# Optimization experiments

Measured on AMD Instinct MI355X. Metric: run time of the kernel, lower is better.

Reference implementation:

```python
import jax, jax.numpy as jnp
import numpy as np

D_MODEL = 1024
N_HEADS = 16
HEAD_DIM = D_MODEL // N_HEADS
LN_EPS = 1e-6


def setup_inputs() -> dict:
    key = jax.random.key(0)
    ks = jax.random.split(key, 10)
    B, L, D = 4, 1024, D_MODEL
    s = 1.0 / np.sqrt(D)
    return {
        "q": jax.random.normal(ks[0], (B, L, D), jnp.float32),
        "k": jax.random.normal(ks[1], (B, L, D), jnp.float32),
        "v": jax.random.normal(ks[2], (B, L, D), jnp.float32),
        "masks": jnp.zeros((B, L, L), jnp.bool_),
        "Wq": jax.random.normal(ks[3], (D, D), jnp.float32) * s,
        "bq": jnp.zeros((D,), jnp.float32),
        "Wk": jax.random.normal(ks[4], (D, D), jnp.float32) * s,
        "bk": jnp.zeros((D,), jnp.float32),
        "Wv": jax.random.normal(ks[5], (D, D), jnp.float32) * s,
        "bv": jnp.zeros((D,), jnp.float32),
        "ln_g": jnp.ones((D,), jnp.float32),
        "ln_b": jnp.zeros((D,), jnp.float32),
    }


def _layer_norm(x, g, b):
    mu = jnp.mean(x, axis=-1, keepdims=True)
    var = jnp.var(x, axis=-1, keepdims=True)
    return (x - mu) * jax.lax.rsqrt(var + LN_EPS) * g + b


def reference(q, k, v, masks, Wq, bq, Wk, bk, Wv, bv, ln_g, ln_b):
    B, Lq, D = q.shape
    Lk = k.shape[1]
    H, Dh = N_HEADS, HEAD_DIM
    # linear projections (nn.Linear: x @ W.T + b)
    qp = q @ Wq.T + bq  # [B, Lq, D]
    kp = k @ Wk.T + bk
    vp = v @ Wv.T + bv
    # split heads: [B, L, D] -> [B, H, L, Dh]
    qh = qp.reshape(B, Lq, H, Dh).transpose(0, 2, 1, 3)
    kh = kp.reshape(B, Lk, H, Dh).transpose(0, 2, 1, 3)
    vh = vp.reshape(B, Lk, H, Dh).transpose(0, 2, 1, 3)
    scores = jnp.einsum("bhqd,bhkd->bhqk", qh, kh) / jnp.sqrt(jnp.float32(Dh))
    scores = jnp.where(masks[:, None, :, :], -jnp.inf, scores)
    attention = jax.nn.softmax(scores, axis=-1)  # [B, H, Lq, Lk]
    ctx = jnp.einsum("bhqk,bhkd->bhqd", attention, vh)  # [B, H, Lq, Dh]
    ctx = ctx.transpose(0, 2, 1, 3).reshape(B, Lq, D)  # unmulti_head
    output = _layer_norm(qp + ctx, ln_g, ln_b)  # residual is projected q
    return output, attention.reshape(B * H, Lq, Lk)
```

## Files before the change

kernel.cpp:

```cpp
#include <hip/hip_runtime.h>
#include <hip/hip_bf16.h>

typedef short bf16x8 __attribute__((ext_vector_type(8)));
typedef short bf16x4 __attribute__((ext_vector_type(4)));
typedef float f32x4 __attribute__((ext_vector_type(4)));
typedef unsigned short u16x8 __attribute__((ext_vector_type(8)));
typedef unsigned short u16x4 __attribute__((ext_vector_type(4)));

#define DEV static __device__ __forceinline__

DEV unsigned short f2bf(float f) {
  unsigned int u = __builtin_bit_cast(unsigned int, f);
  u += 0x7FFFu + ((u >> 16) & 1u);
  return (unsigned short)(u >> 16);
}
DEV float bf2f(unsigned short u) {
  return __builtin_bit_cast(float, (unsigned int)u << 16);
}

DEV void gload_lds16(const unsigned short* g, unsigned short* l) {
  __builtin_amdgcn_global_load_lds(
      (const __attribute__((address_space(1))) unsigned int*)g,
      (__attribute__((address_space(3))) unsigned int*)l, 16, 0, 0);
}

DEV void waitv(int n) {
  switch (n) {
    case 0: asm volatile("s_waitcnt vmcnt(0)" ::: "memory"); break;
    case 1: asm volatile("s_waitcnt vmcnt(1)" ::: "memory"); break;
    case 2: asm volatile("s_waitcnt vmcnt(2)" ::: "memory"); break;
    case 4: asm volatile("s_waitcnt vmcnt(4)" ::: "memory"); break;
    case 6: asm volatile("s_waitcnt vmcnt(6)" ::: "memory"); break;
    default: asm volatile("s_waitcnt vmcnt(0)" ::: "memory"); break;
  }
}

#define SB() __builtin_amdgcn_sched_barrier(0)
#define BAR() do { __builtin_amdgcn_s_barrier(); SB(); } while (0)
#define LBAR() do { asm volatile("s_waitcnt lgkmcnt(0)" ::: "memory"); \
                    SB(); \
                    __builtin_amdgcn_s_barrier(); \
                    SB(); } while (0)
#define WAITL() do { asm volatile("s_waitcnt lgkmcnt(0)" ::: "memory"); SB(); } while (0)
#define PRIO1() __builtin_amdgcn_s_setprio(1)
#define PRIO0() __builtin_amdgcn_s_setprio(0)

__global__ __launch_bounds__(256) void cvt_kernel(
    const float* __restrict__ q, const float* __restrict__ k,
    const float* __restrict__ v, const float* __restrict__ wq,
    const float* __restrict__ wk, const float* __restrict__ wv,
    unsigned short* __restrict__ xq, unsigned short* __restrict__ xk,
    unsigned short* __restrict__ xv, unsigned short* __restrict__ wqb,
    unsigned short* __restrict__ wkb, unsigned short* __restrict__ wvb)
{
  int tid = blockIdx.x * 256 + threadIdx.x;
  const float* src; unsigned short* dst; int off;
  if      (tid <  524288) { src = q;  dst = xq;  off = tid; }
  else if (tid < 1048576) { src = k;  dst = xk;  off = tid -  524288; }
  else if (tid < 1572864) { src = v;  dst = xv;  off = tid - 1048576; }
  else if (tid < 1703936) { src = wq; dst = wqb; off = tid - 1572864; }
  else if (tid < 1835008) { src = wk; dst = wkb; off = tid - 1703936; }
  else                    { src = wv; dst = wvb; off = tid - 1835008; }
  size_t e = (size_t)off * 8;
  float4 a = *(const float4*)(src + e);
  float4 b = *(const float4*)(src + e + 4);
  u16x8 p = { f2bf(a.x), f2bf(a.y), f2bf(a.z), f2bf(a.w),
              f2bf(b.x), f2bf(b.y), f2bf(b.z), f2bf(b.w) };
  *(u16x8*)(dst + e) = p;
}

__global__ __launch_bounds__(512, 2) void gemm_kernel(
    const unsigned short* __restrict__ xq, const unsigned short* __restrict__ xk,
    const unsigned short* __restrict__ xv, const unsigned short* __restrict__ wqb,
    const unsigned short* __restrict__ wkb, const unsigned short* __restrict__ wvb,
    const float* __restrict__ bq, const float* __restrict__ bk,
    const float* __restrict__ bv, unsigned short* __restrict__ qp,
    unsigned short* __restrict__ kp, unsigned short* __restrict__ vt)
{
  __shared__ union {
    unsigned short ab[2][2][128][64];
    unsigned short T[128][132];
  } smu;
  const int t = threadIdx.x, lane = t & 63, wv8 = t >> 6;
  const int ln = lane & 15, g = lane >> 4;
  const int wm2 = wv8 >> 2, wn4 = wv8 & 3;
  const int seg = blockIdx.x >> 8, lb = blockIdx.x & 255;
  const int x8 = lb & 7, s32 = lb >> 3;
  const int m0 = (x8 * 4 + (s32 >> 3)) * 128;
  const int n0 = (s32 & 7) * 128;

  const unsigned short* X; const unsigned short* W; const float* bias;
  unsigned short* outR; int mode;
  if (seg == 0)      { X = xq; W = wqb; bias = bq; outR = qp; mode = 0; }
  else if (seg == 1) { X = xk; W = wkb; bias = bk; outR = kp; mode = 0; }
  else               { X = xv; W = wvb; bias = bv; outR = vt; mode = 2; }

  f32x4 acc[4][2];
#pragma unroll
  for (int i = 0; i < 4; ++i)
#pragma unroll
    for (int j = 0; j < 2; ++j) acc[i][j] = {0.f, 0.f, 0.f, 0.f};

  const int lrow = lane >> 3;
  const int lcol = ((lane & 7) ^ lrow) * 8;

#define STAGE_G(kt) do { \
    const int _k0 = (kt) * 64; \
    _Pragma("unroll") \
    for (int i = 0; i < 2; ++i) { \
      const int r = wv8 * 16 + i * 8; \
      gload_lds16(X + (size_t)(m0 + r + lrow) * 1024 + _k0 + lcol, \
                  &smu.ab[(kt) & 1][0][r][0]); \
      gload_lds16(W + (size_t)(n0 + r + lrow) * 1024 + _k0 + lcol, \
                  &smu.ab[(kt) & 1][1][r][0]); \
    } } while (0)

  STAGE_G(0);
  waitv(0);
  BAR();
#pragma unroll 2
  for (int kt = 0; kt < 16; ++kt) {
    if (kt < 15) STAGE_G(kt + 1);
    SB();
#pragma unroll
    for (int ks = 0; ks < 2; ++ks) {
      bf16x8 af[4], bfr[2];
      const int ru = ((ks * 4 + g) ^ (ln & 7)) * 8;
#pragma unroll
      for (int i = 0; i < 4; ++i)
        af[i] = *(const bf16x8*)&smu.ab[kt & 1][0][wm2 * 64 + i * 16 + ln][ru];
#pragma unroll
      for (int j = 0; j < 2; ++j)
        bfr[j] = *(const bf16x8*)&smu.ab[kt & 1][1][wn4 * 32 + j * 16 + ln][ru];
      PRIO1();
#pragma unroll
      for (int i = 0; i < 4; ++i)
#pragma unroll
        for (int j = 0; j < 2; ++j)
          acc[i][j] = __builtin_amdgcn_mfma_f32_16x16x32_bf16(
              af[i], bfr[j], acc[i][j], 0, 0, 0);
      PRIO0();
    }
    SB();
    waitv(0);
    BAR();
  }

  float bvv[2];
#pragma unroll
  for (int j = 0; j < 2; ++j) bvv[j] = bias[n0 + wn4 * 32 + j * 16 + ln];

  if (mode == 0) {
#pragma unroll
    for (int i = 0; i < 4; ++i)
#pragma unroll
      for (int j = 0; j < 2; ++j)
#pragma unroll
        for (int r = 0; r < 4; ++r) {
          int row = m0 + wm2 * 64 + i * 16 + g * 4 + r;
          int col = n0 + wn4 * 32 + j * 16 + ln;
          outR[(size_t)row * 1024 + col] = f2bf(acc[i][j][r] + bvv[j]);
        }
  } else {
    __syncthreads();
#pragma unroll
    for (int i = 0; i < 4; ++i)
#pragma unroll
      for (int j = 0; j < 2; ++j)
#pragma unroll
        for (int r = 0; r < 4; ++r)
          smu.T[wn4 * 32 + j * 16 + ln][wm2 * 64 + i * 16 + g * 4 + r] =
              f2bf(acc[i][j][r] + bvv[j]);
    __syncthreads();
    const int bb = m0 >> 10, l0 = m0 & 1023;
#pragma unroll
    for (int it = 0; it < 4; ++it) {
      const int col = it * 32 + (t >> 4);
      const int r8 = (t & 15) * 8;
      *(u16x8*)&outR[((size_t)(bb * 16 + (n0 >> 6) + (col >> 6)) * 64 + (col & 63)) * 1024 + l0 + r8] =
          *(const u16x8*)&smu.T[col][r8];
    }
  }
#undef STAGE_G
}

__global__ __launch_bounds__(512, 2) void attn_kernel(
    const unsigned short* __restrict__ qp, const unsigned short* __restrict__ kp,
    const unsigned short* __restrict__ vt, const unsigned char* __restrict__ masks,
    float* __restrict__ attn_out, float* __restrict__ res_out)
{
  __shared__ union {
    unsigned short Kw[8][3][1024];
    unsigned short Vb[3][64][128];
    float ctxp[4][32][68];
  } sm;
  __shared__ float red[2][2][16][4];

  const int t = threadIdx.x;
  const int wv = t >> 6, lane = t & 63;
  const int ln = lane & 15, g = lane >> 4;
  const int wq = wv & 3, wm = wv >> 2;
  const int hw = blockIdx.x;
  const int lid = (hw & 7) * 256 + (hw >> 3);
  const int b = lid >> 9, h = (lid >> 5) & 15, m0 = (lid & 31) * 32;
  const size_t rowbase = (size_t)(b * 1024 + m0);

  bf16x8 qf[2];
  {
    const unsigned short* qb =
        qp + (rowbase + wm * 16 + ln) * 1024 + h * 64 + g * 8;
    qf[0] = *(const bf16x8*)qb;
    qf[1] = *(const bf16x8*)(qb + 32);
  }
  SB();

  const int slr8 = lane >> 3;
  const int suK = (lane & 7) ^ slr8;
  const int vlr = lane >> 4;
  const int vu1 = (lane & 15) ^ vlr;
  const int vu2 = (lane & 15) ^ (4 + vlr);
  const unsigned short* kbase = kp + (size_t)b * 1048576 + h * 64;
  const unsigned short* vtb = vt + ((size_t)(b * 16 + h) * 64) * 1024;
  unsigned short* kwv = &sm.Kw[wv][0][0];

#define STAGE_K(tt) do { \
    gload_lds16(kbase + (size_t)((tt) * 64 + wq * 16 + slr8) * 1024 + suK * 8, \
                kwv + ((tt) % 3) * 1024); \
    gload_lds16(kbase + (size_t)((tt) * 64 + wq * 16 + 8 + slr8) * 1024 + suK * 8, \
                kwv + ((tt) % 3) * 1024 + 512); } while (0)
#define STAGE_V(c) do { \
    gload_lds16(vtb + (size_t)(wv * 8 + vlr) * 1024 + (c) * 128 + vu1 * 8, \
                &sm.Vb[(c) % 3][wv * 8][0]); \
    gload_lds16(vtb + (size_t)(wv * 8 + 4 + vlr) * 1024 + (c) * 128 + vu2 * 8, \
                &sm.Vb[(c) % 3][wv * 8 + 4][0]); } while (0)

  f32x4 sc[16];
#pragma unroll
  for (int i = 0; i < 16; ++i) sc[i] = {0.f, 0.f, 0.f, 0.f};

  STAGE_K(0); STAGE_K(1); STAGE_K(2);
  SB();
#pragma unroll
  for (int tt = 0; tt < 16; ++tt) {
    waitv(tt <= 13 ? 4 : (tt == 14 ? 2 : 0));
    SB();
    const unsigned short* ksl = kwv + (tt % 3) * 1024 + ln * 64;
    bf16x8 kf0 = *(const bf16x8*)(ksl + (g ^ (ln & 7)) * 8);
    bf16x8 kf1 = *(const bf16x8*)(ksl + ((4 + g) ^ (ln & 7)) * 8);
    WAITL();
    if (tt + 3 < 16) STAGE_K(tt + 3);
    SB();
    PRIO1();
    sc[tt] = __builtin_amdgcn_mfma_f32_16x16x32_bf16(kf0, qf[0], sc[tt], 0, 0, 0);
    sc[tt] = __builtin_amdgcn_mfma_f32_16x16x32_bf16(kf1, qf[1], sc[tt], 0, 0, 0);
    PRIO0();
  }

  unsigned mw[16];
  {
    const unsigned char* mrow =
        masks + ((size_t)b * 1024 + m0 + wm * 16 + ln) * 1024 + wq * 16 + g * 4;
#pragma unroll
    for (int tt = 0; tt < 16; ++tt) mw[tt] = *(const unsigned*)(mrow + tt * 64);
  }
  SB();

  LBAR();
  STAGE_V(0); STAGE_V(1);
  SB();

  const float C = 0.18033688011112042f;
  float mx = -3.0e30f;
#pragma unroll
  for (int tt = 0; tt < 16; ++tt) {
    if (mw[tt]) {
#pragma unroll
      for (int r = 0; r < 4; ++r)
        if ((mw[tt] >> (8 * r)) & 0xffu) sc[tt][r] = -1.0e30f;
    }
#pragma unroll
    for (int r = 0; r < 4; ++r) mx = fmaxf(mx, sc[tt][r]);
  }
  mx = fmaxf(mx, __shfl_xor(mx, 16));
  mx = fmaxf(mx, __shfl_xor(mx, 32));
  const float mtl = mx * C;
  float sum = 0.f;
#pragma unroll
  for (int tt = 0; tt < 16; ++tt)
#pragma unroll
    for (int r = 0; r < 4; ++r)
      sum += exp2f(__builtin_fmaf(sc[tt][r], C, -mtl));
  sum += __shfl_xor(sum, 16);
  sum += __shfl_xor(sum, 32);
  if (g == 0) { red[0][wm][ln][wq] = mx; red[1][wm][ln][wq] = sum; }
  LBAR();
  float m4 = fmaxf(fmaxf(red[0][wm][ln][0], red[0][wm][ln][1]),
                   fmaxf(red[0][wm][ln][2], red[0][wm][ln][3]));
  float l4 = 0.f;
#pragma unroll
  for (int i = 0; i < 4; ++i)
    l4 += red[1][wm][ln][i] * exp2f((red[0][wm][ln][i] - m4) * C);
  const float beta = __builtin_fmaf(-m4, C, -__builtin_log2f(l4));

  bf16x8 af8[8];
#pragma unroll
  for (int c = 0; c < 8; ++c) {
    bf16x8 a;
#pragma unroll
    for (int r = 0; r < 4; ++r)
      a[r] = (short)f2bf(exp2f(__builtin_fmaf(sc[2 * c][r], C, beta)));
#pragma unroll
    for (int r = 0; r < 4; ++r)
      a[4 + r] = (short)f2bf(exp2f(__builtin_fmaf(sc[2 * c + 1][r], C, beta)));
    af8[c] = a;
  }

  f32x4 cacc[4];
#pragma unroll
  for (int i = 0; i < 4; ++i) cacc[i] = {0.f, 0.f, 0.f, 0.f};
  const size_t abase =
      ((size_t)(b * 16 + h) * 1024 + (m0 + wm * 16 + ln)) * 1024 + wq * 16 + g * 4;
#pragma unroll
  for (int c = 0; c < 8; ++c) {
    waitv(c == 0 ? 2 : (c == 1 ? 4 : (c <= 6 ? 6 : 4)));
    BAR();
    if (c + 2 < 8) STAGE_V(c + 2);
    SB();
#pragma unroll
    for (int ni = 0; ni < 4; ++ni) {
      const int d = ni * 16 + ln;
      const int u0 = (2 * wq + (g >> 1)) ^ (ln & 7);
      const int u1 = (8 + 2 * wq + (g >> 1)) ^ (ln & 7);
      bf16x4 b0 = *(const bf16x4*)&sm.Vb[c % 3][d][u0 * 8 + (g & 1) * 4];
      bf16x4 b1 = *(const bf16x4*)&sm.Vb[c % 3][d][u1 * 8 + (g & 1) * 4];
      bf16x8 bfr = { b0[0], b0[1], b0[2], b0[3], b1[0], b1[1], b1[2], b1[3] };
      PRIO1();
      cacc[ni] = __builtin_amdgcn_mfma_f32_16x16x32_bf16(af8[c], bfr, cacc[ni], 0, 0, 0);
      PRIO0();
    }
    SB();
#pragma unroll
    for (int hf = 0; hf < 2; ++hf) {
      f32x4 v = { bf2f((unsigned short)af8[c][hf * 4 + 0]),
                  bf2f((unsigned short)af8[c][hf * 4 + 1]),
                  bf2f((unsigned short)af8[c][hf * 4 + 2]),
                  bf2f((unsigned short)af8[c][hf * 4 + 3]) };
      *(f32x4*)(attn_out + abase + (2 * c + hf) * 64) = v;
    }
    SB();
  }

  LBAR();
#pragma unroll
  for (int ni = 0; ni < 4; ++ni)
#pragma unroll
    for (int r = 0; r < 4; ++r)
      sm.ctxp[wq][wm * 16 + g * 4 + r][ni * 16 + ln] = cacc[ni][r];
  LBAR();
  {
    const int m = t >> 4, d4 = (t & 15) * 4;
    f32x4 s0 = *(const f32x4*)&sm.ctxp[0][m][d4];
    f32x4 s1 = *(const f32x4*)&sm.ctxp[1][m][d4];
    f32x4 s2 = *(const f32x4*)&sm.ctxp[2][m][d4];
    f32x4 s3 = *(const f32x4*)&sm.ctxp[3][m][d4];
    f32x4 s = s0 + s1 + s2 + s3;
    const unsigned short* qrow = qp + (rowbase + m) * 1024 + h * 64 + d4;
    u16x4 qv = *(const u16x4*)qrow;
    f32x4 qf32 = { bf2f(qv[0]), bf2f(qv[1]), bf2f(qv[2]), bf2f(qv[3]) };
    s = s + qf32;
    *(f32x4*)(res_out + (rowbase + m) * 1024 + h * 64 + d4) = s;
  }
#undef STAGE_K
#undef STAGE_V
}

__global__ __launch_bounds__(256) void ln_kernel(
    float* __restrict__ io,
    const float* __restrict__ gma, const float* __restrict__ bta)
{
  __shared__ float rbuf[2][4];
  const int r = blockIdx.x, t = threadIdx.x;
  const int i4 = t * 4;
  const size_t base = (size_t)r * 1024 + i4;
  f32x4 x = *(const f32x4*)(io + base);
  float s = x[0] + x[1] + x[2] + x[3];
  float q = x[0]*x[0] + x[1]*x[1] + x[2]*x[2] + x[3]*x[3];
#pragma unroll
  for (int off = 1; off < 64; off <<= 1) {
    s += __shfl_xor(s, off);
    q += __shfl_xor(q, off);
  }
  const int wv = t >> 6;
  if ((t & 63) == 0) { rbuf[0][wv] = s; rbuf[1][wv] = q; }
  __syncthreads();
  s = rbuf[0][0] + rbuf[0][1] + rbuf[0][2] + rbuf[0][3];
  q = rbuf[1][0] + rbuf[1][1] + rbuf[1][2] + rbuf[1][3];
  float mu = s * (1.0f / 1024.0f);
  float var = q * (1.0f / 1024.0f) - mu * mu;
  float is = rsqrtf(var + 1e-6f);
  f32x4 gv = *(const f32x4*)(gma + i4);
  f32x4 bv = *(const f32x4*)(bta + i4);
  f32x4 o;
#pragma unroll
  for (int k = 0; k < 4; ++k) o[k] = (x[k] - mu) * is * gv[k] + bv[k];
  *(f32x4*)(io + base) = o;
}

extern "C" void kernel_launch(void* const* d_in, const int* in_sizes, int n_in,
                              void* d_out, int out_size, void* d_ws, size_t ws_size,
                              hipStream_t stream) {
  const float* q  = (const float*)d_in[0];
  const float* k  = (const float*)d_in[1];
  const float* v  = (const float*)d_in[2];
  const unsigned char* masks = (const unsigned char*)d_in[3];
  const float* Wq = (const float*)d_in[4];
  const float* bq = (const float*)d_in[5];
  const float* Wk = (const float*)d_in[6];
  const float* bk = (const float*)d_in[7];
  const float* Wv = (const float*)d_in[8];
  const float* bv = (const float*)d_in[9];
  const float* lg = (const float*)d_in[10];
  const float* lb = (const float*)d_in[11];

  float* out = (float*)d_out;
  float* attn_out = out + (size_t)4 * 1024 * 1024;

  unsigned short* xq  = (unsigned short*)attn_out;
  unsigned short* xk  = xq + 4194304;
  unsigned short* xv  = xk + 4194304;
  unsigned short* wqb = xv + 4194304;
  unsigned short* wkb = wqb + 1048576;
  unsigned short* wvb = wkb + 1048576;

  unsigned short* qp = (unsigned short*)d_ws;
  unsigned short* kp = qp + 4194304;
  unsigned short* vt = kp + 4194304;

  hipLaunchKernelGGL(cvt_kernel, dim3(7680), dim3(256), 0, stream,
                     q, k, v, Wq, Wk, Wv, xq, xk, xv, wqb, wkb, wvb);
  hipLaunchKernelGGL(gemm_kernel, dim3(768), dim3(512), 0, stream,
                     xq, xk, xv, wqb, wkb, wvb, bq, bk, bv, qp, kp, vt);
  hipLaunchKernelGGL(attn_kernel, dim3(2048), dim3(512), 0, stream,
                     qp, kp, vt, masks, attn_out, out);
  hipLaunchKernelGGL(ln_kernel, dim3(4096), dim3(256), 0, stream,
                     out, lg, lb);
}
```

Baseline: 176.5 us.

## Repartition attention: 16-row blocks, 8 waves split keys, per-wave K/V staging

```diff
diff --git a/kernel.cpp b/kernel.cpp
--- a/kernel.cpp
+++ b/kernel.cpp
@@ -29,7 +29,9 @@
     case 0: asm volatile("s_waitcnt vmcnt(0)" ::: "memory"); break;
     case 1: asm volatile("s_waitcnt vmcnt(1)" ::: "memory"); break;
     case 2: asm volatile("s_waitcnt vmcnt(2)" ::: "memory"); break;
+    case 3: asm volatile("s_waitcnt vmcnt(3)" ::: "memory"); break;
     case 4: asm volatile("s_waitcnt vmcnt(4)" ::: "memory"); break;
+    case 5: asm volatile("s_waitcnt vmcnt(5)" ::: "memory"); break;
     case 6: asm volatile("s_waitcnt vmcnt(6)" ::: "memory"); break;
     default: asm volatile("s_waitcnt vmcnt(0)" ::: "memory"); break;
   }
@@ -44,6 +46,14 @@
 #define WAITL() do { asm volatile("s_waitcnt lgkmcnt(0)" ::: "memory"); SB(); } while (0)
 #define PRIO1() __builtin_amdgcn_s_setprio(1)
 #define PRIO0() __builtin_amdgcn_s_setprio(0)
+
+DEV void amask(unsigned mwv, f32x4& s) {
+  if (mwv) {
+#pragma unroll
+    for (int r = 0; r < 4; ++r)
+      if ((mwv >> (8 * r)) & 0xffu) s[r] = -1.0e30f;
+  }
+}
 
 __global__ __launch_bounds__(256) void cvt_kernel(
     const float* __restrict__ q, const float* __restrict__ k,
@@ -184,31 +194,29 @@
 #undef STAGE_G
 }
 
-__global__ __launch_bounds__(512, 2) void attn_kernel(
+__global__ __launch_bounds__(512, 8) void attn_kernel(
     const unsigned short* __restrict__ qp, const unsigned short* __restrict__ kp,
     const unsigned short* __restrict__ vt, const unsigned char* __restrict__ masks,
     float* __restrict__ attn_out, float* __restrict__ res_out)
 {
   __shared__ union {
-    unsigned short Kw[8][3][1024];
-    unsigned short Vb[3][64][128];
-    float ctxp[4][32][68];
+    unsigned short Kw[8][2][1024];
+    unsigned short Vw[8][3][1024];
+    float ctxp[8][16][68];
   } sm;
-  __shared__ float red[2][2][16][4];
+  __shared__ float red[2][16][8];
 
   const int t = threadIdx.x;
-  const int wv = t >> 6, lane = t & 63;
+  const int wq = t >> 6, lane = t & 63;
   const int ln = lane & 15, g = lane >> 4;
-  const int wq = wv & 3, wm = wv >> 2;
   const int hw = blockIdx.x;
-  const int lid = (hw & 7) * 256 + (hw >> 3);
-  const int b = lid >> 9, h = (lid >> 5) & 15, m0 = (lid & 31) * 32;
+  const int lid = (hw & 7) * 512 + (hw >> 3);
+  const int b = lid >> 10, h = (lid >> 6) & 15, m0 = (lid & 63) * 16;
   const size_t rowbase = (size_t)(b * 1024 + m0);
 
   bf16x8 qf[2];
   {
-    const unsigned short* qb =
-        qp + (rowbase + wm * 16 + ln) * 1024 + h * 64 + g * 8;
+    const unsigned short* qb = qp + (rowbase + ln) * 1024 + h * 64 + g * 8;
     qf[0] = *(const bf16x8*)qb;
     qf[1] = *(const bf16x8*)(qb + 32);
   }
@@ -216,95 +224,92 @@
 
   const int slr8 = lane >> 3;
   const int suK = (lane & 7) ^ slr8;
-  const int vlr = lane >> 4;
-  const int vu1 = (lane & 15) ^ vlr;
-  const int vu2 = (lane & 15) ^ (4 + vlr);
-  const unsigned short* kbase = kp + (size_t)b * 1048576 + h * 64;
-  const unsigned short* vtb = vt + ((size_t)(b * 16 + h) * 64) * 1024;
-  unsigned short* kwv = &sm.Kw[wv][0][0];
-
-#define STAGE_K(tt) do { \
-    gload_lds16(kbase + (size_t)((tt) * 64 + wq * 16 + slr8) * 1024 + suK * 8, \
-                kwv + ((tt) % 3) * 1024); \
-    gload_lds16(kbase + (size_t)((tt) * 64 + wq * 16 + 8 + slr8) * 1024 + suK * 8, \
-                kwv + ((tt) % 3) * 1024 + 512); } while (0)
-#define STAGE_V(c) do { \
-    gload_lds16(vtb + (size_t)(wv * 8 + vlr) * 1024 + (c) * 128 + vu1 * 8, \
-                &sm.Vb[(c) % 3][wv * 8][0]); \
-    gload_lds16(vtb + (size_t)(wv * 8 + 4 + vlr) * 1024 + (c) * 128 + vu2 * 8, \
-                &sm.Vb[(c) % 3][wv * 8 + 4][0]); } while (0)
-
-  f32x4 sc[16];
-#pragma unroll
-  for (int i = 0; i < 16; ++i) sc[i] = {0.f, 0.f, 0.f, 0.f};
-
-  STAGE_K(0); STAGE_K(1); STAGE_K(2);
+  const int vdr = lane >> 1;
+  const int vk8 = (lane & 1) * 8;
+  const unsigned short* kbase =
+      kp + (size_t)b * 1048576 + h * 64 + (size_t)wq * 128 * 1024;
+  const unsigned short* vtb =
+      vt + ((size_t)(b * 16 + h) * 64) * 1024 + wq * 128;
+  unsigned short* kwv = &sm.Kw[wq][0][0];
+  unsigned short* vwv = &sm.Vw[wq][0][0];
+  const unsigned char* mrow =
+      masks + ((size_t)b * 1024 + m0 + ln) * 1024 + wq * 128 + g * 4;
+
+#define STAGE_K(s) do { \
+    gload_lds16(kbase + (size_t)((s) * 16 + slr8) * 1024 + suK * 8, \
+                kwv + ((s) & 1) * 1024); \
+    gload_lds16(kbase + (size_t)((s) * 16 + 8 + slr8) * 1024 + suK * 8, \
+                kwv + ((s) & 1) * 1024 + 512); } while (0)
+#define STAGE_V(s) do { \
+    gload_lds16(vtb + (size_t)vdr * 1024 + (s) * 16 + vk8, \
+                vwv + ((s) % 3) * 1024); \
+    gload_lds16(vtb + (size_t)(32 + vdr) * 1024 + (s) * 16 + vk8, \
+                vwv + ((s) % 3) * 1024 + 512); } while (0)
+
+  f32x4 sc[8];
+#pragma unroll
+  for (int i = 0; i < 8; ++i) sc[i] = {0.f, 0.f, 0.f, 0.f};
+
+  STAGE_K(0); STAGE_K(1);
   SB();
-#pragma unroll
-  for (int tt = 0; tt < 16; ++tt) {
-    waitv(tt <= 13 ? 4 : (tt == 14 ? 2 : 0));
-    SB();
-    const unsigned short* ksl = kwv + (tt % 3) * 1024 + ln * 64;
+  unsigned mq[2];
+#pragma unroll
+  for (int s = 0; s < 8; ++s) {
+    waitv(s == 0 ? 2 : (s == 7 ? 1 : 3));
+    SB();
+    const unsigned short* ksl = kwv + (s & 1) * 1024 + ln * 64;
     bf16x8 kf0 = *(const bf16x8*)(ksl + (g ^ (ln & 7)) * 8);
     bf16x8 kf1 = *(const bf16x8*)(ksl + ((4 + g) ^ (ln & 7)) * 8);
     WAITL();
-    if (tt + 3 < 16) STAGE_K(tt + 3);
-    SB();
+    if (s + 2 < 8) STAGE_K(s + 2);
+    SB();
+    if (s >= 2) amask(mq[s & 1], sc[s - 2]);
+    mq[s & 1] = *(const unsigned*)(mrow + s * 16);
     PRIO1();
-    sc[tt] = __builtin_amdgcn_mfma_f32_16x16x32_bf16(kf0, qf[0], sc[tt], 0, 0, 0);
-    sc[tt] = __builtin_amdgcn_mfma_f32_16x16x32_bf16(kf1, qf[1], sc[tt], 0, 0, 0);
+    sc[s] = __builtin_amdgcn_mfma_f32_16x16x32_bf16(kf0, qf[0], sc[s], 0, 0, 0);
+    sc[s] = __builtin_amdgcn_mfma_f32_16x16x32_bf16(kf1, qf[1], sc[s], 0, 0, 0);
     PRIO0();
   }
-
-  unsigned mw[16];
-  {
-    const unsigned char* mrow =
-        masks + ((size_t)b * 1024 + m0 + wm * 16 + ln) * 1024 + wq * 16 + g * 4;
-#pragma unroll
-    for (int tt = 0; tt < 16; ++tt) mw[tt] = *(const unsigned*)(mrow + tt * 64);
-  }
+  waitv(0);
   SB();
-
-  LBAR();
-  STAGE_V(0); STAGE_V(1);
-  SB();
+  amask(mq[0], sc[6]);
+  amask(mq[1], sc[7]);
 
   const float C = 0.18033688011112042f;
   float mx = -3.0e30f;
 #pragma unroll
-  for (int tt = 0; tt < 16; ++tt) {
-    if (mw[tt]) {
-#pragma unroll
-      for (int r = 0; r < 4; ++r)
-        if ((mw[tt] >> (8 * r)) & 0xffu) sc[tt][r] = -1.0e30f;
-    }
-#pragma unroll
-    for (int r = 0; r < 4; ++r) mx = fmaxf(mx, sc[tt][r]);
-  }
+  for (int s = 0; s < 8; ++s)
+#pragma unroll
+    for (int r = 0; r < 4; ++r) mx = fmaxf(mx, sc[s][r]);
   mx = fmaxf(mx, __shfl_xor(mx, 16));
   mx = fmaxf(mx, __shfl_xor(mx, 32));
   const float mtl = mx * C;
   float sum = 0.f;
 #pragma unroll
-  for (int tt = 0; tt < 16; ++tt)
+  for (int s = 0; s < 8; ++s)
 #pragma unroll
     for (int r = 0; r < 4; ++r)
-      sum += exp2f(__builtin_fmaf(sc[tt][r], C, -mtl));
+      sum += exp2f(__builtin_fmaf(sc[s][r], C, -mtl));
   sum += __shfl_xor(sum, 16);
   sum += __shfl_xor(sum, 32);
-  if (g == 0) { red[0][wm][ln][wq] = mx; red[1][wm][ln][wq] = sum; }
+  if (g == 0) { red[0][ln][wq] = mx; red[1][ln][wq] = sum; }
   LBAR();
-  float m4 = fmaxf(fmaxf(red[0][wm][ln][0], red[0][wm][ln][1]),
-                   fmaxf(red[0][wm][ln][2], red[0][wm][ln][3]));
+
+  STAGE_V(0); STAGE_V(1); STAGE_V(2);
+  SB();
+
+  float m4 = red[0][ln][0];
+#pragma unroll
+  for (int i = 1; i < 8; ++i) m4 = fmaxf(m4, red[0][ln][i]);
   float l4 = 0.f;
 #pragma unroll
-  for (int i = 0; i < 4; ++i)
-    l4 += red[1][wm][ln][i] * exp2f((red[0][wm][ln][i] - m4) * C);
+  for (int i = 0; i < 8; ++i)
+    l4 += red[1][ln][i] * exp2f((red[0][ln][i] - m4) * C);
   const float beta = __builtin_fmaf(-m4, C, -__builtin_log2f(l4));
 
-  bf16x8 af8[8];
-#pragma unroll
-  for (int c = 0; c < 8; ++c) {
+  bf16x8 af[4];
+#pragma unroll
+  for (int c = 0; c < 4; ++c) {
     bf16x8 a;
 #pragma unroll
     for (int r = 0; r < 4; ++r)
@@ -312,40 +317,46 @@
 #pragma unroll
     for (int r = 0; r < 4; ++r)
       a[4 + r] = (short)f2bf(exp2f(__builtin_fmaf(sc[2 * c + 1][r], C, beta)));
-    af8[c] = a;
+    af[c] = a;
   }
 
   f32x4 cacc[4];
 #pragma unroll
   for (int i = 0; i < 4; ++i) cacc[i] = {0.f, 0.f, 0.f, 0.f};
   const size_t abase =
-      ((size_t)(b * 16 + h) * 1024 + (m0 + wm * 16 + ln)) * 1024 + wq * 16 + g * 4;
-#pragma unroll
-  for (int c = 0; c < 8; ++c) {
-    waitv(c == 0 ? 2 : (c == 1 ? 4 : (c <= 6 ? 6 : 4)));
-    BAR();
-    if (c + 2 < 8) STAGE_V(c + 2);
-    SB();
+      ((size_t)(b * 16 + h) * 1024 + (m0 + ln)) * 1024 + wq * 128 + g * 4;
+#pragma unroll
+  for (int p = 0; p < 4; ++p) {
+    waitv(p == 0 ? 2 : (p == 3 ? 2 : 4));
+    SB();
+    bf16x4 b0[4], b1[4];
 #pragma unroll
     for (int ni = 0; ni < 4; ++ni) {
       const int d = ni * 16 + ln;
-      const int u0 = (2 * wq + (g >> 1)) ^ (ln & 7);
-      const int u1 = (8 + 2 * wq + (g >> 1)) ^ (ln & 7);
-      bf16x4 b0 = *(const bf16x4*)&sm.Vb[c % 3][d][u0 * 8 + (g & 1) * 4];
-      bf16x4 b1 = *(const bf16x4*)&sm.Vb[c % 3][d][u1 * 8 + (g & 1) * 4];
-      bf16x8 bfr = { b0[0], b0[1], b0[2], b0[3], b1[0], b1[1], b1[2], b1[3] };
-      PRIO1();
-      cacc[ni] = __builtin_amdgcn_mfma_f32_16x16x32_bf16(af8[c], bfr, cacc[ni], 0, 0, 0);
-      PRIO0();
+      b0[ni] = *(const bf16x4*)(vwv + ((2 * p) % 3) * 1024 + d * 16 + g * 4);
+      b1[ni] = *(const bf16x4*)(vwv + ((2 * p + 1) % 3) * 1024 + d * 16 + g * 4);
     }
+    WAITL();
+    if (p == 0)      { STAGE_V(3); STAGE_V(4); }
+    else if (p == 1) { STAGE_V(5); STAGE_V(6); }
+    else if (p == 2) { STAGE_V(7); }
+    SB();
+    PRIO1();
+#pragma unroll
+    for (int ni = 0; ni < 4; ++ni) {
+      bf16x8 bfr = { b0[ni][0], b0[ni][1], b0[ni][2], b0[ni][3],
+                     b1[ni][0], b1[ni][1], b1[ni][2], b1[ni][3] };
+      cacc[ni] = __builtin_amdgcn_mfma_f32_16x16x32_bf16(af[p], bfr, cacc[ni], 0, 0, 0);
+    }
+    PRIO0();
     SB();
 #pragma unroll
     for (int hf = 0; hf < 2; ++hf) {
-      f32x4 v = { bf2f((unsigned short)af8[c][hf * 4 + 0]),
-                  bf2f((unsigned short)af8[c][hf * 4 + 1]),
-                  bf2f((unsigned short)af8[c][hf * 4 + 2]),
-                  bf2f((unsigned short)af8[c][hf * 4 + 3]) };
-      *(f32x4*)(attn_out + abase + (2 * c + hf) * 64) = v;
+      f32x4 v = { bf2f((unsigned short)af[p][hf * 4 + 0]),
+                  bf2f((unsigned short)af[p][hf * 4 + 1]),
+                  bf2f((unsigned short)af[p][hf * 4 + 2]),
+                  bf2f((unsigned short)af[p][hf * 4 + 3]) };
+      *(f32x4*)(attn_out + abase + p * 32 + hf * 16) = v;
     }
     SB();
   }
@@ -355,15 +366,13 @@
   for (int ni = 0; ni < 4; ++ni)
 #pragma unroll
     for (int r = 0; r < 4; ++r)
-      sm.ctxp[wq][wm * 16 + g * 4 + r][ni * 16 + ln] = cacc[ni][r];
+      sm.ctxp[wq][g * 4 + r][ni * 16 + ln] = cacc[ni][r];
   LBAR();
-  {
+  if (t < 256) {
     const int m = t >> 4, d4 = (t & 15) * 4;
-    f32x4 s0 = *(const f32x4*)&sm.ctxp[0][m][d4];
-    f32x4 s1 = *(const f32x4*)&sm.ctxp[1][m][d4];
-    f32x4 s2 = *(const f32x4*)&sm.ctxp[2][m][d4];
-    f32x4 s3 = *(const f32x4*)&sm.ctxp[3][m][d4];
-    f32x4 s = s0 + s1 + s2 + s3;
+    f32x4 s = *(const f32x4*)&sm.ctxp[0][m][d4];
+#pragma unroll
+    for (int w = 1; w < 8; ++w) s += *(const f32x4*)&sm.ctxp[w][m][d4];
     const unsigned short* qrow = qp + (rowbase + m) * 1024 + h * 64 + d4;
     u16x4 qv = *(const u16x4*)qrow;
     f32x4 qf32 = { bf2f(qv[0]), bf2f(qv[1]), bf2f(qv[2]), bf2f(qv[3]) };
@@ -440,7 +449,7 @@
                      q, k, v, Wq, Wk, Wv, xq, xk, xv, wqb, wkb, wvb);
   hipLaunchKernelGGL(gemm_kernel, dim3(768), dim3(512), 0, stream,
                      xq, xk, xv, wqb, wkb, wvb, bq, bk, bv, qp, kp, vt);
-  hipLaunchKernelGGL(attn_kernel, dim3(2048), dim3(512), 0, stream,
+  hipLaunchKernelGGL(attn_kernel, dim3(4096), dim3(512), 0, stream,
                      qp, kp, vt, masks, attn_out, out);
   hipLaunchKernelGGL(ln_kernel, dim3(4096), dim3(256), 0, stream,
                      out, lg, lb);
```

Result: slower. 201.5 us (+14.2%).

## Split attention into stats+PV kernel and a recompute-and-write attention-probabilities kernel

Applied to the files above, without the earlier changes.

```diff
diff --git a/kernel.cpp b/kernel.cpp
--- a/kernel.cpp
+++ b/kernel.cpp
@@ -29,7 +29,9 @@
     case 0: asm volatile("s_waitcnt vmcnt(0)" ::: "memory"); break;
     case 1: asm volatile("s_waitcnt vmcnt(1)" ::: "memory"); break;
     case 2: asm volatile("s_waitcnt vmcnt(2)" ::: "memory"); break;
+    case 3: asm volatile("s_waitcnt vmcnt(3)" ::: "memory"); break;
     case 4: asm volatile("s_waitcnt vmcnt(4)" ::: "memory"); break;
+    case 5: asm volatile("s_waitcnt vmcnt(5)" ::: "memory"); break;
     case 6: asm volatile("s_waitcnt vmcnt(6)" ::: "memory"); break;
     default: asm volatile("s_waitcnt vmcnt(0)" ::: "memory"); break;
   }
@@ -44,6 +46,14 @@
 #define WAITL() do { asm volatile("s_waitcnt lgkmcnt(0)" ::: "memory"); SB(); } while (0)
 #define PRIO1() __builtin_amdgcn_s_setprio(1)
 #define PRIO0() __builtin_amdgcn_s_setprio(0)
+
+DEV void amask(unsigned mwv, f32x4& s) {
+  if (mwv) {
+#pragma unroll
+    for (int r = 0; r < 4; ++r)
+      if ((mwv >> (8 * r)) & 0xffu) s[r] = -1.0e30f;
+  }
+}
 
 __global__ __launch_bounds__(256) void cvt_kernel(
     const float* __restrict__ q, const float* __restrict__ k,
@@ -184,10 +194,10 @@
 #undef STAGE_G
 }
 
-__global__ __launch_bounds__(512, 2) void attn_kernel(
+__global__ __launch_bounds__(512, 2) void attn_stats_kernel(
     const unsigned short* __restrict__ qp, const unsigned short* __restrict__ kp,
     const unsigned short* __restrict__ vt, const unsigned char* __restrict__ masks,
-    float* __restrict__ attn_out, float* __restrict__ res_out)
+    float* __restrict__ beta_out, float* __restrict__ res_out)
 {
   __shared__ union {
     unsigned short Kw[8][3][1024];
@@ -273,11 +283,7 @@
   float mx = -3.0e30f;
 #pragma unroll
   for (int tt = 0; tt < 16; ++tt) {
-    if (mw[tt]) {
-#pragma unroll
-      for (int r = 0; r < 4; ++r)
-        if ((mw[tt] >> (8 * r)) & 0xffu) sc[tt][r] = -1.0e30f;
-    }
+    amask(mw[tt], sc[tt]);
 #pragma unroll
     for (int r = 0; r < 4; ++r) mx = fmaxf(mx, sc[tt][r]);
   }
@@ -318,11 +324,9 @@
   f32x4 cacc[4];
 #pragma unroll
   for (int i = 0; i < 4; ++i) cacc[i] = {0.f, 0.f, 0.f, 0.f};
-  const size_t abase =
-      ((size_t)(b * 16 + h) * 1024 + (m0 + wm * 16 + ln)) * 1024 + wq * 16 + g * 4;
 #pragma unroll
   for (int c = 0; c < 8; ++c) {
-    waitv(c == 0 ? 2 : (c == 1 ? 4 : (c <= 6 ? 6 : 4)));
+    waitv(c <= 6 ? 2 : 0);
     BAR();
     if (c + 2 < 8) STAGE_V(c + 2);
     SB();
@@ -339,16 +343,10 @@
       PRIO0();
     }
     SB();
-#pragma unroll
-    for (int hf = 0; hf < 2; ++hf) {
-      f32x4 v = { bf2f((unsigned short)af8[c][hf * 4 + 0]),
-                  bf2f((unsigned short)af8[c][hf * 4 + 1]),
-                  bf2f((unsigned short)af8[c][hf * 4 + 2]),
-                  bf2f((unsigned short)af8[c][hf * 4 + 3]) };
-      *(f32x4*)(attn_out + abase + (2 * c + hf) * 64) = v;
-    }
-    SB();
-  }
+  }
+
+  if (g == 0 && wq == 0)
+    beta_out[(size_t)(b * 16 + h) * 1024 + m0 + wm * 16 + ln] = beta;
 
   LBAR();
 #pragma unroll
@@ -374,6 +372,90 @@
 #undef STAGE_V
 }
 
+__global__ __launch_bounds__(512, 2) void attn_write_kernel(
+    const unsigned short* __restrict__ qp, const unsigned short* __restrict__ kp,
+    const unsigned char* __restrict__ masks, const float* __restrict__ beta_arr,
+    float* __restrict__ attn_out)
+{
+  __shared__ unsigned short Kw[8][3][1024];
+
+  const int t = threadIdx.x;
+  const int wv = t >> 6, lane = t & 63;
+  const int ln = lane & 15, g = lane >> 4;
+  const int wq = wv & 3, wm = wv >> 2;
+  const int hw = blockIdx.x;
+  const int lid = (hw & 7) * 256 + (hw >> 3);
+  const int b = lid >> 9, h = (lid >> 5) & 15, m0 = (lid & 31) * 32;
+  const size_t rowbase = (size_t)(b * 1024 + m0);
+
+  bf16x8 qf[2];
+  {
+    const unsigned short* qb =
+        qp + (rowbase + wm * 16 + ln) * 1024 + h * 64 + g * 8;
+    qf[0] = *(const bf16x8*)qb;
+    qf[1] = *(const bf16x8*)(qb + 32);
+  }
+  SB();
+
+  const int slr8 = lane >> 3;
+  const int suK = (lane & 7) ^ slr8;
+  const unsigned short* kbase = kp + (size_t)b * 1048576 + h * 64;
+  unsigned short* kwv = &Kw[wv][0][0];
+
+#define STAGE_K(tt) do { \
+    gload_lds16(kbase + (size_t)((tt) * 64 + wq * 16 + slr8) * 1024 + suK * 8, \
+                kwv + ((tt) % 3) * 1024); \
+    gload_lds16(kbase + (size_t)((tt) * 64 + wq * 16 + 8 + slr8) * 1024 + suK * 8, \
+                kwv + ((tt) % 3) * 1024 + 512); } while (0)
+
+  f32x4 sc[16];
+#pragma unroll
+  for (int i = 0; i < 16; ++i) sc[i] = {0.f, 0.f, 0.f, 0.f};
+
+  STAGE_K(0); STAGE_K(1); STAGE_K(2);
+  SB();
+#pragma unroll
+  for (int tt = 0; tt < 16; ++tt) {
+    waitv(tt <= 13 ? 4 : (tt == 14 ? 2 : 0));
+    SB();
+    const unsigned short* ksl = kwv + (tt % 3) * 1024 + ln * 64;
+    bf16x8 kf0 = *(const bf16x8*)(ksl + (g ^ (ln & 7)) * 8);
+    bf16x8 kf1 = *(const bf16x8*)(ksl + ((4 + g) ^ (ln & 7)) * 8);
+    WAITL();
+    if (tt + 3 < 16) STAGE_K(tt + 3);
+    SB();
+    PRIO1();
+    sc[tt] = __builtin_amdgcn_mfma_f32_16x16x32_bf16(kf0, qf[0], sc[tt], 0, 0, 0);
+    sc[tt] = __builtin_amdgcn_mfma_f32_16x16x32_bf16(kf1, qf[1], sc[tt], 0, 0, 0);
+    PRIO0();
+  }
+
+  unsigned mw[16];
+  {
+    const unsigned char* mrow =
+        masks + ((size_t)b * 1024 + m0 + wm * 16 + ln) * 1024 + wq * 16 + g * 4;
+#pragma unroll
+    for (int tt = 0; tt < 16; ++tt) mw[tt] = *(const unsigned*)(mrow + tt * 64);
+  }
+  const float beta = beta_arr[(size_t)(b * 16 + h) * 1024 + m0 + wm * 16 + ln];
+  waitv(0);
+  SB();
+
+  const float C = 0.18033688011112042f;
+  const size_t abase =
+      ((size_t)(b * 16 + h) * 1024 + (m0 + wm * 16 + ln)) * 1024 + wq * 16 + g * 4;
+#pragma unroll
+  for (int tt = 0; tt < 16; ++tt) {
+    amask(mw[tt], sc[tt]);
+    f32x4 v;
+#pragma unroll
+    for (int r = 0; r < 4; ++r)
+      v[r] = exp2f(__builtin_fmaf(sc[tt][r], C, beta));
+    *(f32x4*)(attn_out + abase + tt * 64) = v;
+  }
+#undef STAGE_K
+}
+
 __global__ __launch_bounds__(256) void ln_kernel(
     float* __restrict__ io,
     const float* __restrict__ gma, const float* __restrict__ bta)
@@ -435,13 +517,16 @@
   unsigned short* qp = (unsigned short*)d_ws;
   unsigned short* kp = qp + 4194304;
   unsigned short* vt = kp + 4194304;
+  float* beta = (float*)(vt + 4194304);
 
   hipLaunchKernelGGL(cvt_kernel, dim3(7680), dim3(256), 0, stream,
                      q, k, v, Wq, Wk, Wv, xq, xk, xv, wqb, wkb, wvb);
   hipLaunchKernelGGL(gemm_kernel, dim3(768), dim3(512), 0, stream,
                      xq, xk, xv, wqb, wkb, wvb, bq, bk, bv, qp, kp, vt);
-  hipLaunchKernelGGL(attn_kernel, dim3(2048), dim3(512), 0, stream,
-                     qp, kp, vt, masks, attn_out, out);
+  hipLaunchKernelGGL(attn_stats_kernel, dim3(2048), dim3(512), 0, stream,
+                     qp, kp, vt, masks, beta, out);
+  hipLaunchKernelGGL(attn_write_kernel, dim3(2048), dim3(512), 0, stream,
+                     qp, kp, masks, beta, attn_out);
   hipLaunchKernelGGL(ln_kernel, dim3(4096), dim3(256), 0, stream,
                      out, lg, lb);
 }
```

Result: slower. 233.8 us (+32.5%).
